# Kernel optimization log

Hardware: AMD Instinct MI355X
Metric: run time of the kernel (lower is better)

Reference implementation:

```python
import jax, jax.numpy as jnp
import numpy as np

S = 4          # num species
E = 8          # ensemble members (num_batched_networks)
N = 50000      # atoms (single conformer)
AEV = 1008     # aev_dim
ALPHA = 0.1    # CELU alpha (torchani default)
DIMS = [AEV, 256, 192, 160, 1]


def setup_inputs() -> dict:
    key = jax.random.key(0)
    ks = jax.random.split(key, 9)
    # species with exactly N/S atoms per element, randomly permuted
    rs = np.random.RandomState(0)
    sp = np.repeat(np.arange(S), N // S)
    rs.shuffle(sp)
    species = jnp.asarray(sp.reshape(1, N), dtype=jnp.int32)
    # static per-species index lists (equal sizes -> stackable), mirrors cached idx_list
    idx = np.stack([np.nonzero(sp == i)[0] for i in range(S)]).astype(np.int32)  # [S, N//S]
    aev = jax.random.normal(ks[0], (1, N, AEV), dtype=jnp.float32)
    inp = {"aev": aev, "species": species, "idx": jnp.asarray(idx)}
    # per-species, per-ensemble-member weights: W [S,E,din,dout], b [S,E,1,dout]
    for li in range(4):
        din, dout = DIMS[li], DIMS[li + 1]
        kw = jax.random.fold_in(ks[1], li)
        kb = jax.random.fold_in(ks[2], li)
        inp[f"W{li+1}"] = jax.random.normal(kw, (S, E, din, dout), dtype=jnp.float32) / np.sqrt(din).astype(np.float32)
        inp[f"b{li+1}"] = jax.random.normal(kb, (S, E, 1, dout), dtype=jnp.float32) * 0.1
    return inp


def reference(aev, W1, b1, W2, b2, W3, b3, W4, b4, species, idx):
    x = aev.reshape(-1, AEV)                       # flatten(0,1): [N, AEV]
    energies = jnp.zeros((x.shape[0],), dtype=x.dtype)
    celu = lambda v: jax.nn.celu(v, alpha=ALPHA)
    for i in range(S):                              # loop over species (small, static)
        xi = x[idx[i]]                              # gather: [n_i, AEV]
        # BmmAtomicNetwork: expand over ensemble dim, baddbmm chain + CELU
        h = celu(jnp.einsum('ni,eio->eno', xi, W1[i]) + b1[i])   # [E, n_i, 256]
        h = celu(jnp.einsum('eni,eio->eno', h, W2[i]) + b2[i])   # [E, n_i, 192]
        h = celu(jnp.einsum('eni,eio->eno', h, W3[i]) + b3[i])   # [E, n_i, 160]
        h = jnp.einsum('eni,eio->eno', h, W4[i]) + b4[i]          # [E, n_i, 1]
        energies = energies.at[idx[i]].set(h.mean(axis=0).reshape(-1))  # scatter
    # forward: squeeze(0) then sum(0, keepdim=True) -> molecular energy [1]
    return jnp.sum(energies, keepdims=True)
```

## Files before the change

### kernel.cpp

```cpp
#include <hip/hip_runtime.h>

#define S_    4
#define E_    8
#define NPS   12500
#define AEVD  1008
#define D1    256
#define D2    192
#define D3    160
#define TM    64
#define NT    ((NPS + TM - 1) / TM)
#define TG    8
#define NG    ((NT + TG - 1) / TG)
#define ALPHA 0.1f
#define RS    1024
#define NROW  (NT * TM)

#define KB1 32
#define NB1 16
#define KB2 8
#define NB2 12
#define KB3 6
#define NB3 10

typedef __attribute__((ext_vector_type(8))) short short8;
typedef __attribute__((ext_vector_type(4))) float f32x4;

__device__ __forceinline__ ushort f2bf(float f) {
    unsigned u = __float_as_uint(f);
    unsigned r = u + 0x7FFFu + ((u >> 16) & 1u);
    return (ushort)(r >> 16);
}
__device__ __forceinline__ float celu_f(float v) {
    return v > 0.0f ? v : ALPHA * (__expf(v * (1.0f / ALPHA)) - 1.0f);
}
__device__ __forceinline__ void sync_lds() {
    asm volatile("s_waitcnt lgkmcnt(0)" ::: "memory");
    __builtin_amdgcn_s_barrier();
}
#define GLD16(g, lp) __builtin_amdgcn_global_load_lds( \
    (const __attribute__((address_space(1))) void*)(g), \
    (__attribute__((address_space(3))) void*)(lp), 16, 0, 0)

__device__ __forceinline__ void pack_body(const float* __restrict__ W, ushort* __restrict__ out,
                                          int Ksrc, int kbs, int nbs, int Nsrc, int b)
{
    const int kb = b % kbs;
    const int se = b / kbs;
    const int t  = threadIdx.x;
    const int l  = t & 63, q = t >> 6;
    const float* Wse = W + (size_t)se * Ksrc * Nsrc;
    for (int i = 0; i < 4; ++i) {
        int nb = q + i * 4;
        if (nb >= nbs) break;
        int n = nb * 16 + (l & 15);
        ushort v[8];
        #pragma unroll
        for (int j = 0; j < 8; ++j) {
            int k = kb * 32 + ((l >> 4) << 3) + j;
            float x = (k < Ksrc) ? Wse[(size_t)k * Nsrc + n] : 0.0f;
            v[j] = f2bf(x);
        }
        uint4 u;
        u.x = (unsigned)v[0] | ((unsigned)v[1] << 16);
        u.y = (unsigned)v[2] | ((unsigned)v[3] << 16);
        u.z = (unsigned)v[4] | ((unsigned)v[5] << 16);
        u.w = (unsigned)v[6] | ((unsigned)v[7] << 16);
        *(uint4*)(out + ((((size_t)se * kbs + kb) * nbs + nb) * 64 + l) * 8) = u;
    }
}

#define PACKB (S_ * E_ * (KB1 + KB2 + KB3))
#define GATBS (NROW * (RS / 8) / 256)
#define GATB  (GATBS * S_)

__global__ void prep(const float* __restrict__ W1, const float* __restrict__ W2,
                     const float* __restrict__ W3,
                     ushort* __restrict__ o1, ushort* __restrict__ o2, ushort* __restrict__ o3,
                     const float* __restrict__ aev, const int* __restrict__ idx,
                     ushort* __restrict__ aevb)
{
    int b = blockIdx.x;
    if (b < S_ * E_ * KB1)                  { pack_body(W1, o1, AEVD, KB1, NB1, D1, b); return; }
    b -= S_ * E_ * KB1;
    if (b < S_ * E_ * KB2)                  { pack_body(W2, o2, D1,   KB2, NB2, D2, b); return; }
    b -= S_ * E_ * KB2;
    if (b < S_ * E_ * KB3)                  { pack_body(W3, o3, D2,   KB3, NB3, D3, b); return; }
    b -= S_ * E_ * KB3;
    const int s    = b / GATBS;
    const int r    = (b % GATBS) * 256 + threadIdx.x;
    const int grow = r >> 7;
    const int k0   = (r & 127) << 3;
    uint4 u = {0u, 0u, 0u, 0u};
    if (grow < NPS && k0 < AEVD) {
        const float* src = aev + (size_t)idx[s * NPS + grow] * AEVD + k0;
        float4 a = *(const float4*)(src);
        float4 c = *(const float4*)(src + 4);
        u.x = (unsigned)f2bf(a.x) | ((unsigned)f2bf(a.y) << 16);
        u.y = (unsigned)f2bf(a.z) | ((unsigned)f2bf(a.w) << 16);
        u.z = (unsigned)f2bf(c.x) | ((unsigned)f2bf(c.y) << 16);
        u.w = (unsigned)f2bf(c.z) | ((unsigned)f2bf(c.w) << 16);
    }
    *(uint4*)(aevb + ((size_t)s * NROW + grow) * RS + k0) = u;
}

__device__ __forceinline__ float layers234(ushort* hrow, int se, int l, int kq,
                                           const ushort* __restrict__ W2p,
                                           const ushort* __restrict__ W3p,
                                           const float* __restrict__ b2,
                                           const float* __restrict__ b3,
                                           const float* __restrict__ W4)
{
    const ushort* w2se = W2p + (size_t)se * (KB2 * NB2 * 512);
    f32x4 acc2[NB2];
    #pragma unroll
    for (int i = 0; i < NB2; ++i) acc2[i] = (f32x4){0.f, 0.f, 0.f, 0.f};

    #pragma unroll
    for (int ch = 0; ch < 2; ++ch) {
        const int mb0 = ch * 6;
        uint4 A0[6], A1[6];
        auto AL2 = [&](int kb, int i) {
            return *(const uint4*)(w2se + ((size_t)(kb * NB2 + (mb0 + i)) * 64 + l) * 8);
        };
        #pragma unroll
        for (int i = 0; i < 6; ++i) A0[i] = AL2(0, i);
        short8 bf0 = *(const short8*)(hrow + 0 * 32 + kq * 8);
        #pragma unroll
        for (int kb = 0; kb < KB2; kb += 2) {
            short8 bf1 = *(const short8*)(hrow + (kb + 1) * 32 + kq * 8);
            #pragma unroll
            for (int i = 0; i < 6; ++i) A1[i] = AL2(kb + 1, i);
            #pragma unroll
            for (int i = 0; i < 6; ++i)
                acc2[mb0 + i] = __builtin_amdgcn_mfma_f32_16x16x32_bf16(*(short8*)&A0[i], bf0, acc2[mb0 + i], 0, 0, 0);
            if (kb + 2 < KB2) {
                bf0 = *(const short8*)(hrow + (kb + 2) * 32 + kq * 8);
                #pragma unroll
                for (int i = 0; i < 6; ++i) A0[i] = AL2(kb + 2, i);
            }
            #pragma unroll
            for (int i = 0; i < 6; ++i)
                acc2[mb0 + i] = __builtin_amdgcn_mfma_f32_16x16x32_bf16(*(short8*)&A1[i], bf1, acc2[mb0 + i], 0, 0, 0);
        }
    }
    #pragma unroll
    for (int mb = 0; mb < NB2; ++mb) {
        float4 bv = *(const float4*)&b2[se * D2 + mb * 16 + kq * 4];
        uint2 u;
        u.x = (unsigned)f2bf(celu_f(acc2[mb][0] + bv.x)) | ((unsigned)f2bf(celu_f(acc2[mb][1] + bv.y)) << 16);
        u.y = (unsigned)f2bf(celu_f(acc2[mb][2] + bv.z)) | ((unsigned)f2bf(celu_f(acc2[mb][3] + bv.w)) << 16);
        *(uint2*)(hrow + mb * 16 + kq * 4) = u;
    }

    const ushort* w3se = W3p + (size_t)se * (KB3 * NB3 * 512);
    f32x4 acc3[NB3];
    #pragma unroll
    for (int i = 0; i < NB3; ++i) acc3[i] = (f32x4){0.f, 0.f, 0.f, 0.f};

    #pragma unroll
    for (int ch = 0; ch < 2; ++ch) {
        const int mb0 = ch * 5;
        uint4 A0[5], A1[5];
        auto AL3 = [&](int kb, int i) {
            return *(const uint4*)(w3se + ((size_t)(kb * NB3 + (mb0 + i)) * 64 + l) * 8);
        };
        #pragma unroll
        for (int i = 0; i < 5; ++i) A0[i] = AL3(0, i);
        short8 bf0 = *(const short8*)(hrow + 0 * 32 + kq * 8);
        #pragma unroll
        for (int kb = 0; kb < KB3; kb += 2) {
            short8 bf1 = *(const short8*)(hrow + (kb + 1) * 32 + kq * 8);
            #pragma unroll
            for (int i = 0; i < 5; ++i) A1[i] = AL3(kb + 1, i);
            #pragma unroll
            for (int i = 0; i < 5; ++i)
                acc3[mb0 + i] = __builtin_amdgcn_mfma_f32_16x16x32_bf16(*(short8*)&A0[i], bf0, acc3[mb0 + i], 0, 0, 0);
            if (kb + 2 < KB3) {
                bf0 = *(const short8*)(hrow + (kb + 2) * 32 + kq * 8);
                #pragma unroll
                for (int i = 0; i < 5; ++i) A0[i] = AL3(kb + 2, i);
            }
            #pragma unroll
            for (int i = 0; i < 5; ++i)
                acc3[mb0 + i] = __builtin_amdgcn_mfma_f32_16x16x32_bf16(*(short8*)&A1[i], bf1, acc3[mb0 + i], 0, 0, 0);
        }
    }

    float e = 0.0f;
    #pragma unroll
    for (int mb = 0; mb < NB3; ++mb) {
        float4 b3v = *(const float4*)&b3[se * D3 + mb * 16 + kq * 4];
        float4 w4v = *(const float4*)&W4[se * D3 + mb * 16 + kq * 4];
        e += celu_f(acc3[mb][0] + b3v.x) * w4v.x;
        e += celu_f(acc3[mb][1] + b3v.y) * w4v.y;
        e += celu_f(acc3[mb][2] + b3v.z) * w4v.z;
        e += celu_f(acc3[mb][3] + b3v.w) * w4v.w;
    }
    return e;
}

__global__ __launch_bounds__(256, 3)
void ani_mfma(const ushort* __restrict__ aevb,
              const ushort* __restrict__ W1p, const ushort* __restrict__ W2p,
              const ushort* __restrict__ W3p,
              const float* __restrict__ b1, const float* __restrict__ b2,
              const float* __restrict__ b3,
              const float* __restrict__ W4, const float* __restrict__ b4,
              float* __restrict__ partials)
{
    const int se   = blockIdx.x & 31;
    const int ti   = blockIdx.x >> 5;
    const int tile = blockIdx.y * TG + ti;
    if (tile >= NT) return;
    const int s = se >> 3;
    const int t = threadIdx.x;
    const int w = t >> 6, l = t & 63;
    const int lm = l & 15, kq = l >> 4;
    const int swz = (kq ^ ((lm >> 1) & 3)) << 3;

    __shared__ ushort H1s[TM][D1 + 8];
    __shared__ __align__(16) ushort Ast[2][TM][32];

    const int aL  = l >> 2;
    const int gch = (l & 3) ^ ((l >> 3) & 3);
    const ushort* gsrc = aevb + ((size_t)s * NROW + (size_t)tile * TM + w * 16 + aL) * RS + gch * 8;
    ushort* lbase0 = &Ast[0][w * 16][0];
    ushort* lbase1 = &Ast[1][w * 16][0];

    const ushort* w1se = W1p + (size_t)se * (KB1 * NB1 * 512);
    const ushort* bptr = w1se + ((size_t)(w * 4) * 64 + l) * 8;

    f32x4 acc1[4][4];
    #pragma unroll
    for (int mi = 0; mi < 4; ++mi)
        #pragma unroll
        for (int j = 0; j < 4; ++j) acc1[mi][j] = (f32x4){0.f, 0.f, 0.f, 0.f};

    uint4 B0[4], B1[4];
    auto loadB = [&](uint4* Bt, int kb) {
        #pragma unroll
        for (int i = 0; i < 4; ++i)
            Bt[i] = *(const uint4*)(bptr + (size_t)kb * (NB1 * 512) + i * 512);
    };
    auto mfma16 = [&](const ushort (*Ab)[32], uint4* Bt) {
        #pragma unroll
        for (int mi = 0; mi < 4; ++mi) {
            short8 af = *(const short8*)&Ab[mi * 16 + lm][swz];
            #pragma unroll
            for (int j = 0; j < 4; ++j)
                acc1[mi][j] = __builtin_amdgcn_mfma_f32_16x16x32_bf16(af, *(short8*)&Bt[j], acc1[mi][j], 0, 0, 0);
        }
    };

    GLD16(gsrc, lbase0);
    loadB(B0, 0);
    for (int kb = 0; kb < KB1; kb += 2) {
        asm volatile("s_waitcnt vmcnt(4)" ::: "memory");
        __builtin_amdgcn_s_barrier();
        GLD16(gsrc + (kb + 1) * 32, lbase1);
        loadB(B1, kb + 1);
        mfma16(Ast[0], B0);
        asm volatile("s_waitcnt vmcnt(4)" ::: "memory");
        __builtin_amdgcn_s_barrier();
        if (kb + 2 < KB1) {
            GLD16(gsrc + (kb + 2) * 32, lbase0);
            loadB(B0, kb + 2);
        }
        mfma16(Ast[1], B1);
    }
    #pragma unroll
    for (int j = 0; j < 4; ++j) {
        int n = (w * 4 + j) * 16 + lm;
        float bias = b1[se * D1 + n];
        #pragma unroll
        for (int mi = 0; mi < 4; ++mi)
            #pragma unroll
            for (int r = 0; r < 4; ++r)
                H1s[mi * 16 + kq * 4 + r][n] = f2bf(celu_f(acc1[mi][j][r] + bias));
    }
    sync_lds();

    ushort* hrow = &H1s[w * 16 + lm][0];
    float e = layers234(hrow, se, l, kq, W2p, W3p, b2, b3, W4);

    if (tile * TM + w * 16 + lm >= NPS) e = 0.0f;
    #pragma unroll
    for (int o = 32; o > 0; o >>= 1) e += __shfl_xor(e, o);

    float* red = (float*)&Ast[0][0][0];
    if (l == 0) red[w] = e;
    __syncthreads();
    if (t == 0) {
        int nv = NPS - tile * TM; if (nv > TM) nv = TM;
        partials[tile * (S_ * E_) + se] = red[0] + red[1] + red[2] + red[3] + (float)nv * b4[se];
    }
}

__global__ __launch_bounds__(256, 3)
void ani_mfma_fb(const float* __restrict__ aev, const int* __restrict__ idx,
                 const ushort* __restrict__ W1p, const ushort* __restrict__ W2p,
                 const ushort* __restrict__ W3p,
                 const float* __restrict__ b1, const float* __restrict__ b2,
                 const float* __restrict__ b3,
                 const float* __restrict__ W4, const float* __restrict__ b4,
                 float* __restrict__ partials)
{
    const int se   = blockIdx.x & 31;
    const int ti   = blockIdx.x >> 5;
    const int tile = blockIdx.y * TG + ti;
    if (tile >= NT) return;
    const int s = se >> 3;
    const int t = threadIdx.x;
    const int w = t >> 6, l = t & 63;
    const int lm = l & 15, kq = l >> 4;

    __shared__ ushort H1s[TM][D1 + 8];
    __shared__ __align__(16) ushort Ast[2][4][TM][8];

    const int srow = tile * TM + l;
    const int src  = srow < NPS ? srow : NPS - 1;
    const float* arowp = aev + (size_t)idx[s * NPS + src] * AEVD;
    const int wo = w * 8;

    const ushort* w1se = W1p + (size_t)se * (KB1 * NB1 * 512);

    f32x4 acc1[4][4];
    #pragma unroll
    for (int mi = 0; mi < 4; ++mi)
        #pragma unroll
        for (int j = 0; j < 4; ++j) acc1[mi][j] = (f32x4){0.f, 0.f, 0.f, 0.f};

    uint4 B0[4], B1[4];
    float4 na, nbv;

    auto loadB = [&](uint4* Bt, int kb) {
        #pragma unroll
        for (int i = 0; i < 4; ++i)
            Bt[i] = *(const uint4*)(w1se + ((size_t)(kb * NB1 + (w * 4 + i)) * 64 + l) * 8);
    };
    auto stageA = [&](int kbw) {
        short8 v;
        v[0] = (short)f2bf(na.x);  v[1] = (short)f2bf(na.y);
        v[2] = (short)f2bf(na.z);  v[3] = (short)f2bf(na.w);
        v[4] = (short)f2bf(nbv.x); v[5] = (short)f2bf(nbv.y);
        v[6] = (short)f2bf(nbv.z); v[7] = (short)f2bf(nbv.w);
        *(short8*)&Ast[kbw & 1][w][l][0] = v;
        if (kbw + 1 < KB1) {
            int ko = (kbw + 1) * 32 + wo;
            if (ko > AEVD - 8) ko = AEVD - 8;
            na  = *(const float4*)(arowp + ko);
            nbv = *(const float4*)(arowp + ko + 4);
        }
    };
    auto mfma16 = [&](int buf, uint4* Bt) {
        #pragma unroll
        for (int mi = 0; mi < 4; ++mi) {
            short8 af = *(const short8*)&Ast[buf][kq][mi * 16 + lm][0];
            #pragma unroll
            for (int j = 0; j < 4; ++j)
                acc1[mi][j] = __builtin_amdgcn_mfma_f32_16x16x32_bf16(af, *(short8*)&Bt[j], acc1[mi][j], 0, 0, 0);
        }
    };

    {
        float4 ca = *(const float4*)(arowp + wo);
        float4 cb = *(const float4*)(arowp + wo + 4);
        short8 v;
        v[0] = (short)f2bf(ca.x); v[1] = (short)f2bf(ca.y);
        v[2] = (short)f2bf(ca.z); v[3] = (short)f2bf(ca.w);
        v[4] = (short)f2bf(cb.x); v[5] = (short)f2bf(cb.y);
        v[6] = (short)f2bf(cb.z); v[7] = (short)f2bf(cb.w);
        *(short8*)&Ast[0][w][l][0] = v;
        na  = *(const float4*)(arowp + 32 + wo);
        nbv = *(const float4*)(arowp + 32 + wo + 4);
        loadB(B0, 0);
        loadB(B1, 1);
        sync_lds();
    }

    for (int kb = 0; kb < KB1; kb += 2) {
        if (kb + 1 < KB1) stageA(kb + 1);
        mfma16(0, B0);
        if (kb + 2 < KB1) loadB(B0, kb + 2);
        sync_lds();
        if (kb + 2 < KB1) stageA(kb + 2);
        mfma16(1, B1);
        if (kb + 3 < KB1) loadB(B1, kb + 3);
        sync_lds();
    }
    #pragma unroll
    for (int j = 0; j < 4; ++j) {
        int n = (w * 4 + j) * 16 + lm;
        float bias = b1[se * D1 + n];
        #pragma unroll
        for (int mi = 0; mi < 4; ++mi)
            #pragma unroll
            for (int r = 0; r < 4; ++r)
                H1s[mi * 16 + kq * 4 + r][n] = f2bf(celu_f(acc1[mi][j][r] + bias));
    }
    sync_lds();

    ushort* hrow = &H1s[w * 16 + lm][0];
    float e = layers234(hrow, se, l, kq, W2p, W3p, b2, b3, W4);

    if (tile * TM + w * 16 + lm >= NPS) e = 0.0f;
    #pragma unroll
    for (int o = 32; o > 0; o >>= 1) e += __shfl_xor(e, o);

    float* red = (float*)&Ast[0][0][0][0];
    if (l == 0) red[w] = e;
    __syncthreads();
    if (t == 0) {
        int nv = NPS - tile * TM; if (nv > TM) nv = TM;
        partials[tile * (S_ * E_) + se] = red[0] + red[1] + red[2] + red[3] + (float)nv * b4[se];
    }
}

__global__ void reduce_partials(const float* __restrict__ p, int n, float* __restrict__ out)
{
    float s = 0.0f;
    for (int i = threadIdx.x; i < n; i += 256) s += p[i];
    #pragma unroll
    for (int o = 32; o > 0; o >>= 1) s += __shfl_xor(s, o);
    __shared__ float sm[4];
    if ((threadIdx.x & 63) == 0) sm[threadIdx.x >> 6] = s;
    __syncthreads();
    if (threadIdx.x == 0) out[0] = (sm[0] + sm[1] + sm[2] + sm[3]) * (1.0f / E_);
}

extern "C" void kernel_launch(void* const* d_in, const int* in_sizes, int n_in,
                              void* d_out, int out_size, void* d_ws, size_t ws_size,
                              hipStream_t stream)
{
    const float* aev = (const float*)d_in[0];
    const int*   idx = (const int*)  d_in[2];
    const float* W1  = (const float*)d_in[3];
    const float* b1  = (const float*)d_in[4];
    const float* W2  = (const float*)d_in[5];
    const float* b2  = (const float*)d_in[6];
    const float* W3  = (const float*)d_in[7];
    const float* b3  = (const float*)d_in[8];
    const float* W4  = (const float*)d_in[9];
    const float* b4  = (const float*)d_in[10];
    float* out = (float*)d_out;

    ushort* w1p = (ushort*)d_ws;
    ushort* w2p = w1p + (size_t)S_ * E_ * KB1 * NB1 * 512;
    ushort* w3p = w2p + (size_t)S_ * E_ * KB2 * NB2 * 512;
    float* partials = (float*)(w3p + (size_t)S_ * E_ * KB3 * NB3 * 512);
    ushort* aevb = (ushort*)(partials + NT * S_ * E_);

    const size_t aevb_bytes = (size_t)S_ * NROW * RS * sizeof(ushort);
    const size_t need = ((char*)aevb - (char*)d_ws) + aevb_bytes;

    dim3 grid(32 * TG, NG);

    if (ws_size >= need) {
        prep<<<PACKB + GATB, 256, 0, stream>>>(W1, W2, W3, w1p, w2p, w3p, aev, idx, aevb);
        ani_mfma<<<grid, 256, 0, stream>>>(aevb, w1p, w2p, w3p,
                                           b1, b2, b3, W4, b4, partials);
    } else {
        prep<<<PACKB, 256, 0, stream>>>(W1, W2, W3, w1p, w2p, w3p, aev, idx, (ushort*)partials);
        ani_mfma_fb<<<grid, 256, 0, stream>>>(aev, idx, w1p, w2p, w3p,
                                              b1, b2, b3, W4, b4, partials);
    }
    reduce_partials<<<1, 256, 0, stream>>>(partials, NT * S_ * E_, out);
}
```

Baseline: 721.2 us.

## Restructure layers 2-3 as block-wide MFMA tiling with swizzled shared activations

Layers 2 and 3 change from a per-wave 16-row tile that loaded every weight column block to a block-wide scheme. Each wave now owns a slice of output column blocks across all 64 rows and reads activations from a swizzled, unpadded shared-memory buffer. Each weight fragment is loaded once per block instead of once per wave, which cuts global/L2 weight traffic, and the XOR swizzle is meant to avoid LDS bank conflicts. In exchange, layer 3 wastes MFMA work on padded column blocks (12 computed for 10 needed), needs extra barriers, and a cross-wave shared-memory reduction; the fallback kernel for small workspaces is removed.

```diff
diff --git a/kernel.cpp b/kernel.cpp
--- a/kernel.cpp
+++ b/kernel.cpp
@@ -103,102 +103,6 @@
     *(uint4*)(aevb + ((size_t)s * NROW + grow) * RS + k0) = u;
 }
 
-__device__ __forceinline__ float layers234(ushort* hrow, int se, int l, int kq,
-                                           const ushort* __restrict__ W2p,
-                                           const ushort* __restrict__ W3p,
-                                           const float* __restrict__ b2,
-                                           const float* __restrict__ b3,
-                                           const float* __restrict__ W4)
-{
-    const ushort* w2se = W2p + (size_t)se * (KB2 * NB2 * 512);
-    f32x4 acc2[NB2];
-    #pragma unroll
-    for (int i = 0; i < NB2; ++i) acc2[i] = (f32x4){0.f, 0.f, 0.f, 0.f};
-
-    #pragma unroll
-    for (int ch = 0; ch < 2; ++ch) {
-        const int mb0 = ch * 6;
-        uint4 A0[6], A1[6];
-        auto AL2 = [&](int kb, int i) {
-            return *(const uint4*)(w2se + ((size_t)(kb * NB2 + (mb0 + i)) * 64 + l) * 8);
-        };
-        #pragma unroll
-        for (int i = 0; i < 6; ++i) A0[i] = AL2(0, i);
-        short8 bf0 = *(const short8*)(hrow + 0 * 32 + kq * 8);
-        #pragma unroll
-        for (int kb = 0; kb < KB2; kb += 2) {
-            short8 bf1 = *(const short8*)(hrow + (kb + 1) * 32 + kq * 8);
-            #pragma unroll
-            for (int i = 0; i < 6; ++i) A1[i] = AL2(kb + 1, i);
-            #pragma unroll
-            for (int i = 0; i < 6; ++i)
-                acc2[mb0 + i] = __builtin_amdgcn_mfma_f32_16x16x32_bf16(*(short8*)&A0[i], bf0, acc2[mb0 + i], 0, 0, 0);
-            if (kb + 2 < KB2) {
-                bf0 = *(const short8*)(hrow + (kb + 2) * 32 + kq * 8);
-                #pragma unroll
-                for (int i = 0; i < 6; ++i) A0[i] = AL2(kb + 2, i);
-            }
-            #pragma unroll
-            for (int i = 0; i < 6; ++i)
-                acc2[mb0 + i] = __builtin_amdgcn_mfma_f32_16x16x32_bf16(*(short8*)&A1[i], bf1, acc2[mb0 + i], 0, 0, 0);
-        }
-    }
-    #pragma unroll
-    for (int mb = 0; mb < NB2; ++mb) {
-        float4 bv = *(const float4*)&b2[se * D2 + mb * 16 + kq * 4];
-        uint2 u;
-        u.x = (unsigned)f2bf(celu_f(acc2[mb][0] + bv.x)) | ((unsigned)f2bf(celu_f(acc2[mb][1] + bv.y)) << 16);
-        u.y = (unsigned)f2bf(celu_f(acc2[mb][2] + bv.z)) | ((unsigned)f2bf(celu_f(acc2[mb][3] + bv.w)) << 16);
-        *(uint2*)(hrow + mb * 16 + kq * 4) = u;
-    }
-
-    const ushort* w3se = W3p + (size_t)se * (KB3 * NB3 * 512);
-    f32x4 acc3[NB3];
-    #pragma unroll
-    for (int i = 0; i < NB3; ++i) acc3[i] = (f32x4){0.f, 0.f, 0.f, 0.f};
-
-    #pragma unroll
-    for (int ch = 0; ch < 2; ++ch) {
-        const int mb0 = ch * 5;
-        uint4 A0[5], A1[5];
-        auto AL3 = [&](int kb, int i) {
-            return *(const uint4*)(w3se + ((size_t)(kb * NB3 + (mb0 + i)) * 64 + l) * 8);
-        };
-        #pragma unroll
-        for (int i = 0; i < 5; ++i) A0[i] = AL3(0, i);
-        short8 bf0 = *(const short8*)(hrow + 0 * 32 + kq * 8);
-        #pragma unroll
-        for (int kb = 0; kb < KB3; kb += 2) {
-            short8 bf1 = *(const short8*)(hrow + (kb + 1) * 32 + kq * 8);
-            #pragma unroll
-            for (int i = 0; i < 5; ++i) A1[i] = AL3(kb + 1, i);
-            #pragma unroll
-            for (int i = 0; i < 5; ++i)
-                acc3[mb0 + i] = __builtin_amdgcn_mfma_f32_16x16x32_bf16(*(short8*)&A0[i], bf0, acc3[mb0 + i], 0, 0, 0);
-            if (kb + 2 < KB3) {
-                bf0 = *(const short8*)(hrow + (kb + 2) * 32 + kq * 8);
-                #pragma unroll
-                for (int i = 0; i < 5; ++i) A0[i] = AL3(kb + 2, i);
-            }
-            #pragma unroll
-            for (int i = 0; i < 5; ++i)
-                acc3[mb0 + i] = __builtin_amdgcn_mfma_f32_16x16x32_bf16(*(short8*)&A1[i], bf1, acc3[mb0 + i], 0, 0, 0);
-        }
-    }
-
-    float e = 0.0f;
-    #pragma unroll
-    for (int mb = 0; mb < NB3; ++mb) {
-        float4 b3v = *(const float4*)&b3[se * D3 + mb * 16 + kq * 4];
-        float4 w4v = *(const float4*)&W4[se * D3 + mb * 16 + kq * 4];
-        e += celu_f(acc3[mb][0] + b3v.x) * w4v.x;
-        e += celu_f(acc3[mb][1] + b3v.y) * w4v.y;
-        e += celu_f(acc3[mb][2] + b3v.z) * w4v.z;
-        e += celu_f(acc3[mb][3] + b3v.w) * w4v.w;
-    }
-    return e;
-}
-
 __global__ __launch_bounds__(256, 3)
 void ani_mfma(const ushort* __restrict__ aevb,
               const ushort* __restrict__ W1p, const ushort* __restrict__ W2p,
@@ -218,7 +122,7 @@
     const int lm = l & 15, kq = l >> 4;
     const int swz = (kq ^ ((lm >> 1) & 3)) << 3;
 
-    __shared__ ushort H1s[TM][D1 + 8];
+    __shared__ ushort H1s[TM * D1];
     __shared__ __align__(16) ushort Ast[2][TM][32];
 
     const int aL  = l >> 2;
@@ -275,144 +179,152 @@
         #pragma unroll
         for (int mi = 0; mi < 4; ++mi)
             #pragma unroll
-            for (int r = 0; r < 4; ++r)
-                H1s[mi * 16 + kq * 4 + r][n] = f2bf(celu_f(acc1[mi][j][r] + bias));
+            for (int r = 0; r < 4; ++r) {
+                int row = mi * 16 + kq * 4 + r;
+                H1s[row * D1 + (n ^ ((4 * (kq & 1) + r) << 3))] = f2bf(celu_f(acc1[mi][j][r] + bias));
+            }
     }
     sync_lds();
 
-    ushort* hrow = &H1s[w * 16 + lm][0];
-    float e = layers234(hrow, se, l, kq, W2p, W3p, b2, b3, W4);
-
-    if (tile * TM + w * 16 + lm >= NPS) e = 0.0f;
-    #pragma unroll
-    for (int o = 32; o > 0; o >>= 1) e += __shfl_xor(e, o);
+    const int hxA = (lm & 7) << 3;
+    const int nbase = w * 3;
+    const ushort* w2se = W2p + (size_t)se * (KB2 * NB2 * 512);
+
+    f32x4 acc2[4][3];
+    #pragma unroll
+    for (int mi = 0; mi < 4; ++mi)
+        #pragma unroll
+        for (int i = 0; i < 3; ++i) acc2[mi][i] = (f32x4){0.f, 0.f, 0.f, 0.f};
+
+    {
+        uint4 Wb0[3], Wb1[3];
+        short8 Ah0[4], Ah1[4];
+        auto LW2 = [&](uint4* d, int kb) {
+            #pragma unroll
+            for (int i = 0; i < 3; ++i)
+                d[i] = *(const uint4*)(w2se + ((size_t)(kb * NB2 + nbase + i) * 64 + l) * 8);
+        };
+        auto LA1 = [&](short8* d, int kb) {
+            #pragma unroll
+            for (int mi = 0; mi < 4; ++mi)
+                d[mi] = *(const short8*)&H1s[(mi * 16 + lm) * D1 + ((kb * 32 + kq * 8) ^ hxA)];
+        };
+        LW2(Wb0, 0); LA1(Ah0, 0);
+        #pragma unroll
+        for (int kb = 0; kb < KB2; kb += 2) {
+            LW2(Wb1, kb + 1); LA1(Ah1, kb + 1);
+            #pragma unroll
+            for (int mi = 0; mi < 4; ++mi)
+                #pragma unroll
+                for (int i = 0; i < 3; ++i)
+                    acc2[mi][i] = __builtin_amdgcn_mfma_f32_16x16x32_bf16(Ah0[mi], *(short8*)&Wb0[i], acc2[mi][i], 0, 0, 0);
+            if (kb + 2 < KB2) { LW2(Wb0, kb + 2); LA1(Ah0, kb + 2); }
+            #pragma unroll
+            for (int mi = 0; mi < 4; ++mi)
+                #pragma unroll
+                for (int i = 0; i < 3; ++i)
+                    acc2[mi][i] = __builtin_amdgcn_mfma_f32_16x16x32_bf16(Ah1[mi], *(short8*)&Wb1[i], acc2[mi][i], 0, 0, 0);
+        }
+    }
+    __syncthreads();
+
+    ushort* H2 = H1s;
+    #pragma unroll
+    for (int i = 0; i < 3; ++i) {
+        int n2 = (nbase + i) * 16 + lm;
+        float bias = b2[se * D2 + n2];
+        #pragma unroll
+        for (int mi = 0; mi < 4; ++mi)
+            #pragma unroll
+            for (int r = 0; r < 4; ++r) {
+                int row = mi * 16 + kq * 4 + r;
+                H2[row * D2 + (n2 ^ ((4 * (kq & 1) + r) << 3))] = f2bf(celu_f(acc2[mi][i][r] + bias));
+            }
+    }
+    __syncthreads();
+
+    const ushort* w3se = W3p + (size_t)se * (KB3 * NB3 * 512);
+
+    f32x4 acc3[4][3];
+    #pragma unroll
+    for (int mi = 0; mi < 4; ++mi)
+        #pragma unroll
+        for (int i = 0; i < 3; ++i) acc3[mi][i] = (f32x4){0.f, 0.f, 0.f, 0.f};
+
+    {
+        uint4 Wc0[3], Wc1[3];
+        short8 Bh0[4], Bh1[4];
+        auto LW3 = [&](uint4* d, int kb) {
+            #pragma unroll
+            for (int i = 0; i < 3; ++i) {
+                int nb = nbase + i; nb = nb < NB3 ? nb : NB3 - 1;
+                d[i] = *(const uint4*)(w3se + ((size_t)(kb * NB3 + nb) * 64 + l) * 8);
+            }
+        };
+        auto LA2 = [&](short8* d, int kb) {
+            #pragma unroll
+            for (int mi = 0; mi < 4; ++mi)
+                d[mi] = *(const short8*)&H2[(mi * 16 + lm) * D2 + ((kb * 32 + kq * 8) ^ hxA)];
+        };
+        LW3(Wc0, 0); LA2(Bh0, 0);
+        #pragma unroll
+        for (int kb = 0; kb < KB3; kb += 2) {
+            LW3(Wc1, kb + 1); LA2(Bh1, kb + 1);
+            #pragma unroll
+            for (int mi = 0; mi < 4; ++mi)
+                #pragma unroll
+                for (int i = 0; i < 3; ++i)
+                    acc3[mi][i] = __builtin_amdgcn_mfma_f32_16x16x32_bf16(Bh0[mi], *(short8*)&Wc0[i], acc3[mi][i], 0, 0, 0);
+            if (kb + 2 < KB3) { LW3(Wc0, kb + 2); LA2(Bh0, kb + 2); }
+            #pragma unroll
+            for (int mi = 0; mi < 4; ++mi)
+                #pragma unroll
+                for (int i = 0; i < 3; ++i)
+                    acc3[mi][i] = __builtin_amdgcn_mfma_f32_16x16x32_bf16(Bh1[mi], *(short8*)&Wc1[i], acc3[mi][i], 0, 0, 0);
+        }
+    }
+
+    f32x4 s0 = {0,0,0,0}, s1 = {0,0,0,0}, s2 = {0,0,0,0}, s3 = {0,0,0,0};
+    #pragma unroll
+    for (int i = 0; i < 3; ++i) {
+        bool valid = (nbase + i) < NB3;
+        int n3 = (valid ? (nbase + i) : 0) * 16 + lm;
+        float bv = valid ? b3[se * D3 + n3] : 0.f;
+        float wv = valid ? W4[se * D3 + n3] : 0.f;
+        #pragma unroll
+        for (int r = 0; r < 4; ++r) {
+            s0[r] += celu_f(acc3[0][i][r] + bv) * wv;
+            s1[r] += celu_f(acc3[1][i][r] + bv) * wv;
+            s2[r] += celu_f(acc3[2][i][r] + bv) * wv;
+            s3[r] += celu_f(acc3[3][i][r] + bv) * wv;
+        }
+    }
+    #pragma unroll
+    for (int o = 1; o <= 8; o <<= 1) {
+        #pragma unroll
+        for (int r = 0; r < 4; ++r) {
+            s0[r] += __shfl_xor(s0[r], o);
+            s1[r] += __shfl_xor(s1[r], o);
+            s2[r] += __shfl_xor(s2[r], o);
+            s3[r] += __shfl_xor(s3[r], o);
+        }
+    }
+    f32x4 sm = (lm & 8) ? ((lm & 4) ? s3 : s2) : ((lm & 4) ? s1 : s0);
+    float v = (lm & 2) ? ((lm & 1) ? sm[3] : sm[2]) : ((lm & 1) ? sm[1] : sm[0]);
 
     float* red = (float*)&Ast[0][0][0];
-    if (l == 0) red[w] = e;
+    red[w * 64 + (lm >> 2) * 16 + kq * 4 + (lm & 3)] = v;
     __syncthreads();
-    if (t == 0) {
-        int nv = NPS - tile * TM; if (nv > TM) nv = TM;
-        partials[tile * (S_ * E_) + se] = red[0] + red[1] + red[2] + red[3] + (float)nv * b4[se];
-    }
-}
-
-__global__ __launch_bounds__(256, 3)
-void ani_mfma_fb(const float* __restrict__ aev, const int* __restrict__ idx,
-                 const ushort* __restrict__ W1p, const ushort* __restrict__ W2p,
-                 const ushort* __restrict__ W3p,
-                 const float* __restrict__ b1, const float* __restrict__ b2,
-                 const float* __restrict__ b3,
-                 const float* __restrict__ W4, const float* __restrict__ b4,
-                 float* __restrict__ partials)
-{
-    const int se   = blockIdx.x & 31;
-    const int ti   = blockIdx.x >> 5;
-    const int tile = blockIdx.y * TG + ti;
-    if (tile >= NT) return;
-    const int s = se >> 3;
-    const int t = threadIdx.x;
-    const int w = t >> 6, l = t & 63;
-    const int lm = l & 15, kq = l >> 4;
-
-    __shared__ ushort H1s[TM][D1 + 8];
-    __shared__ __align__(16) ushort Ast[2][4][TM][8];
-
-    const int srow = tile * TM + l;
-    const int src  = srow < NPS ? srow : NPS - 1;
-    const float* arowp = aev + (size_t)idx[s * NPS + src] * AEVD;
-    const int wo = w * 8;
-
-    const ushort* w1se = W1p + (size_t)se * (KB1 * NB1 * 512);
-
-    f32x4 acc1[4][4];
-    #pragma unroll
-    for (int mi = 0; mi < 4; ++mi)
-        #pragma unroll
-        for (int j = 0; j < 4; ++j) acc1[mi][j] = (f32x4){0.f, 0.f, 0.f, 0.f};
-
-    uint4 B0[4], B1[4];
-    float4 na, nbv;
-
-    auto loadB = [&](uint4* Bt, int kb) {
-        #pragma unroll
-        for (int i = 0; i < 4; ++i)
-            Bt[i] = *(const uint4*)(w1se + ((size_t)(kb * NB1 + (w * 4 + i)) * 64 + l) * 8);
-    };
-    auto stageA = [&](int kbw) {
-        short8 v;
-        v[0] = (short)f2bf(na.x);  v[1] = (short)f2bf(na.y);
-        v[2] = (short)f2bf(na.z);  v[3] = (short)f2bf(na.w);
-        v[4] = (short)f2bf(nbv.x); v[5] = (short)f2bf(nbv.y);
-        v[6] = (short)f2bf(nbv.z); v[7] = (short)f2bf(nbv.w);
-        *(short8*)&Ast[kbw & 1][w][l][0] = v;
-        if (kbw + 1 < KB1) {
-            int ko = (kbw + 1) * 32 + wo;
-            if (ko > AEVD - 8) ko = AEVD - 8;
-            na  = *(const float4*)(arowp + ko);
-            nbv = *(const float4*)(arowp + ko + 4);
-        }
-    };
-    auto mfma16 = [&](int buf, uint4* Bt) {
-        #pragma unroll
-        for (int mi = 0; mi < 4; ++mi) {
-            short8 af = *(const short8*)&Ast[buf][kq][mi * 16 + lm][0];
-            #pragma unroll
-            for (int j = 0; j < 4; ++j)
-                acc1[mi][j] = __builtin_amdgcn_mfma_f32_16x16x32_bf16(af, *(short8*)&Bt[j], acc1[mi][j], 0, 0, 0);
-        }
-    };
-
-    {
-        float4 ca = *(const float4*)(arowp + wo);
-        float4 cb = *(const float4*)(arowp + wo + 4);
-        short8 v;
-        v[0] = (short)f2bf(ca.x); v[1] = (short)f2bf(ca.y);
-        v[2] = (short)f2bf(ca.z); v[3] = (short)f2bf(ca.w);
-        v[4] = (short)f2bf(cb.x); v[5] = (short)f2bf(cb.y);
-        v[6] = (short)f2bf(cb.z); v[7] = (short)f2bf(cb.w);
-        *(short8*)&Ast[0][w][l][0] = v;
-        na  = *(const float4*)(arowp + 32 + wo);
-        nbv = *(const float4*)(arowp + 32 + wo + 4);
-        loadB(B0, 0);
-        loadB(B1, 1);
-        sync_lds();
-    }
-
-    for (int kb = 0; kb < KB1; kb += 2) {
-        if (kb + 1 < KB1) stageA(kb + 1);
-        mfma16(0, B0);
-        if (kb + 2 < KB1) loadB(B0, kb + 2);
-        sync_lds();
-        if (kb + 2 < KB1) stageA(kb + 2);
-        mfma16(1, B1);
-        if (kb + 3 < KB1) loadB(B1, kb + 3);
-        sync_lds();
-    }
-    #pragma unroll
-    for (int j = 0; j < 4; ++j) {
-        int n = (w * 4 + j) * 16 + lm;
-        float bias = b1[se * D1 + n];
-        #pragma unroll
-        for (int mi = 0; mi < 4; ++mi)
-            #pragma unroll
-            for (int r = 0; r < 4; ++r)
-                H1s[mi * 16 + kq * 4 + r][n] = f2bf(celu_f(acc1[mi][j][r] + bias));
-    }
-    sync_lds();
-
-    ushort* hrow = &H1s[w * 16 + lm][0];
-    float e = layers234(hrow, se, l, kq, W2p, W3p, b2, b3, W4);
-
-    if (tile * TM + w * 16 + lm >= NPS) e = 0.0f;
-    #pragma unroll
-    for (int o = 32; o > 0; o >>= 1) e += __shfl_xor(e, o);
-
-    float* red = (float*)&Ast[0][0][0][0];
-    if (l == 0) red[w] = e;
-    __syncthreads();
-    if (t == 0) {
-        int nv = NPS - tile * TM; if (nv > TM) nv = TM;
-        partials[tile * (S_ * E_) + se] = red[0] + red[1] + red[2] + red[3] + (float)nv * b4[se];
+    if (t < 64) {
+        int a = t;
+        float e = red[a] + red[64 + a] + red[128 + a] + red[192 + a];
+        if (tile * TM + a >= NPS) e = 0.0f;
+        #pragma unroll
+        for (int o = 32; o > 0; o >>= 1) e += __shfl_xor(e, o);
+        if (t == 0) {
+            int nv = NPS - tile * TM; if (nv > TM) nv = TM;
+            partials[tile * (S_ * E_) + se] = e + (float)nv * b4[se];
+        }
     }
 }
 
@@ -450,19 +362,10 @@
     float* partials = (float*)(w3p + (size_t)S_ * E_ * KB3 * NB3 * 512);
     ushort* aevb = (ushort*)(partials + NT * S_ * E_);
 
-    const size_t aevb_bytes = (size_t)S_ * NROW * RS * sizeof(ushort);
-    const size_t need = ((char*)aevb - (char*)d_ws) + aevb_bytes;
+    prep<<<PACKB + GATB, 256, 0, stream>>>(W1, W2, W3, w1p, w2p, w3p, aev, idx, aevb);
 
     dim3 grid(32 * TG, NG);
-
-    if (ws_size >= need) {
-        prep<<<PACKB + GATB, 256, 0, stream>>>(W1, W2, W3, w1p, w2p, w3p, aev, idx, aevb);
-        ani_mfma<<<grid, 256, 0, stream>>>(aevb, w1p, w2p, w3p,
-                                           b1, b2, b3, W4, b4, partials);
-    } else {
-        prep<<<PACKB, 256, 0, stream>>>(W1, W2, W3, w1p, w2p, w3p, aev, idx, (ushort*)partials);
-        ani_mfma_fb<<<grid, 256, 0, stream>>>(aev, idx, w1p, w2p, w3p,
-                                              b1, b2, b3, W4, b4, partials);
-    }
+    ani_mfma<<<grid, 256, 0, stream>>>(aevb, w1p, w2p, w3p,
+                                       b1, b2, b3, W4, b4, partials);
     reduce_partials<<<1, 256, 0, stream>>>(partials, NT * S_ * E_, out);
 }
```

Result: faster. 666.8 us (-7.6%).
